# Performance work log

Hardware: AMD Instinct MI355X
Metric: run time of the kernel (lower is better)

## Reference

```python
import math
import jax, jax.numpy as jnp
import numpy as np

B, N, L, E, H, T = 64, 8, 128, 768, 12, 64


def setup_inputs() -> dict:
    key = jax.random.key(0)
    ks = jax.random.split(key, 8)
    s = 0.02
    return {
        "x":  jax.random.normal(ks[0], (B, N, L, E), dtype=jnp.float32),
        # torch Linear weights are [out, in]
        "Wq": jax.random.normal(ks[1], (H, E, E), dtype=jnp.float32) * s,
        "bq": jax.random.normal(ks[2], (H, E), dtype=jnp.float32) * s,
        "Wv": jax.random.normal(ks[3], (H, T, E), dtype=jnp.float32) * s,
        "bv": jax.random.normal(ks[4], (H, T), dtype=jnp.float32) * s,
        "Wf": jax.random.normal(ks[5], (E, H * T), dtype=jnp.float32) * s,
        "bf": jax.random.normal(ks[6], (E,), dtype=jnp.float32) * s,
    }


def reference(x, Wq, bq, Wv, bv, Wf, bf):
    b, n, l, e = x.shape
    S = b * n                      # set_size after the view(-1, L, E)
    x2 = x.reshape(S, l, e)
    # per-head query projection (batched over heads)
    Q = jnp.einsum('sle,hfe->hslf', x2, Wq) + bq[:, None, None, :]      # [H,S,L,E]
    # raw (unsoftmaxed) attention: (Q K^T) V / sqrt(E)
    scores = jnp.einsum('hslf,smf->hslm', Q, x2)                        # [H,S,L,L]
    attn = jnp.einsum('hslm,sme->hsle', scores, x2) * (1.0 / math.sqrt(e))
    # per-head value projection to transformer_dim
    V = jnp.einsum('hsle,hte->hslt', attn, Wv) + bv[:, None, None, :]   # [H,S,L,T]
    # concat heads along last dim (head order preserved)
    cat = jnp.transpose(V, (1, 2, 0, 3)).reshape(S, l, -1)              # [S,L,H*T]
    out = cat @ Wf.T + bf                                               # [S,L,E]
    return out.reshape(b, n, l, e)
```

## Files before the change

kernel.cpp:

```cpp
#include <hip/hip_runtime.h>
#include <stdint.h>


#define EE 768
#define SLOT 50331648L

typedef short s16x8 __attribute__((ext_vector_type(8)));
typedef float f32x4 __attribute__((ext_vector_type(4)));

__device__ __forceinline__ short f2bf(float f){
  union { float fv; uint32_t u; } v; v.fv = f;
  uint32_t r = (v.u + 0x7fffu + ((v.u >> 16) & 1u)) >> 16;
  return (short)r;
}

__device__ __forceinline__ void gld_lds16(const short* g, short* l){
  __builtin_amdgcn_global_load_lds(
      (const __attribute__((address_space(1))) void*)(uintptr_t)g,
      (__attribute__((address_space(3))) void*)(uintptr_t)l,
      16, 0, 0);
}

__device__ __forceinline__ int xcd_swz(int bid, int nwg){
  int xcd = bid & 7, loc = bid >> 3;
  int q = nwg >> 3, r = nwg & 7;
  return (xcd < r ? xcd * (q + 1) : r * (q + 1) + (xcd - r) * q) + loc;
}

__device__ __forceinline__ int swz64(int row, int c){ return c ^ ((row & 7) << 3); }
__device__ __forceinline__ int swz32(int row, int c){ return c ^ (((row >> 1) & 3) << 3); }

__global__ __launch_bounds__(256) void cast_bf16_k(const float* __restrict__ src,
                                                   short* __restrict__ dst,
                                                   long n, float scale){
  long i = ((long)blockIdx.x * 256 + threadIdx.x) * 8;
  if(i >= n) return;
  float4 a = *(const float4*)(src + i);
  float4 b = *(const float4*)(src + i + 4);
  s16x8 o;
  o[0]=f2bf(a.x*scale); o[1]=f2bf(a.y*scale); o[2]=f2bf(a.z*scale); o[3]=f2bf(a.w*scale);
  o[4]=f2bf(b.x*scale); o[5]=f2bf(b.y*scale); o[6]=f2bf(b.z*scale); o[7]=f2bf(b.w*scale);
  *(s16x8*)(dst + i) = o;
}

__global__ __launch_bounds__(256) void cvec_k(const float* __restrict__ Wf,
                                              const float* __restrict__ bv,
                                              const float* __restrict__ bfv,
                                              float* __restrict__ c){
  int e = blockIdx.x * 256 + threadIdx.x;
  if(e >= EE) return;
  float s = bfv[e];
  for(int k = 0; k < EE; ++k) s += Wf[(long)e * EE + k] * bv[k];
  c[e] = s;
}

__global__ __launch_bounds__(256) void bias_build(const float* __restrict__ bq,
                                                  float* __restrict__ biasQP){
  int i = blockIdx.x * 256 + threadIdx.x;
  if(i < 9984) biasQP[i] = (i < 9216) ? bq[i] : 0.f;
}

__global__ __launch_bounds__(512, 1) void gemm256(const short* __restrict__ A,
                                                  const short* __restrict__ W,
                                                  const float* __restrict__ bias,
                                                  short* __restrict__ OutBase,
                                                  int hBase, int nSub, int pSub){
  __shared__ short lds[2][16384];
  const int tid = threadIdx.x, lane = tid & 63, w = tid >> 6;
  const int wr = w >> 2, wc = w & 3;
  const int bid = xcd_swz(blockIdx.x, nSub * 768);
  const int g = bid / 768, rb = bid - g * 768;
  const int rowBlk = rb / 3, colBlk = rb - rowBlk * 3;
  const long rowA0 = (long)rowBlk * 256;
  const int colB0 = colBlk * 256;
  const int wh = (g == pSub) ? 12 : hBase + g;
  const short* Bm = W + (long)wh * 589824L;
  short* Out = OutBase + (long)g * SLOT;

  const int sr0 = w * 32 + (lane >> 2);
  const int sr1 = sr0 + 16;
  const int scol = (lane & 3) * 8;
  const int sc0 = swz32(sr0, scol);
  const int sc1 = swz32(sr1, scol);
  const short* Ar0 = A + (rowA0 + sr0) * 768;
  const short* Ar1 = A + (rowA0 + sr1) * 768;
  const short* Br0 = Bm + (long)(colB0 + sr0) * 768;
  const short* Br1 = Bm + (long)(colB0 + sr1) * 768;

  f32x4 acc[8][4] = {};
  s16x8 af[4], bf0[2], bf1[2];
  const int fr = lane & 15, fc = (lane >> 4) * 8;

  auto stage = [&](int b, int kt){
    short* Al = &lds[b][0];
    short* Bl = &lds[b][8192];
    gld_lds16(Ar0 + kt + sc0, Al + (w * 2) * 512);
    gld_lds16(Ar1 + kt + sc1, Al + (w * 2 + 1) * 512);
    gld_lds16(Br0 + kt + sc0, Bl + (w * 2) * 512);
    gld_lds16(Br1 + kt + sc1, Bl + (w * 2 + 1) * 512);
  };

  stage(0, 0);
  for(int t = 0; t < 24; ++t){
    if(t < 23){
      stage((t + 1) & 1, (t + 1) * 32);
      asm volatile("s_waitcnt vmcnt(4)\n\ts_barrier" ::: "memory");
    } else {
      asm volatile("s_waitcnt vmcnt(0)\n\ts_barrier" ::: "memory");
    }
    const short* Al = &lds[t & 1][0];
    const short* Bl = &lds[t & 1][8192];

    auto loadA = [&](int mh){
      #pragma unroll
      for(int m = 0; m < 4; ++m){
        int row = wr * 128 + (mh * 4 + m) * 16 + fr;
        af[m] = *(const s16x8*)&Al[row * 32 + swz32(row, fc)];
      }
    };
    auto loadB = [&](int nh, s16x8* bf){
      #pragma unroll
      for(int n = 0; n < 2; ++n){
        int row = wc * 64 + (nh * 2 + n) * 16 + fr;
        bf[n] = *(const s16x8*)&Bl[row * 32 + swz32(row, fc)];
      }
    };
    auto mm = [&](int mh, int nh, s16x8* bf){
      __builtin_amdgcn_s_setprio(1);
      #pragma unroll
      for(int m = 0; m < 4; ++m)
        #pragma unroll
        for(int n = 0; n < 2; ++n)
          acc[mh * 4 + m][nh * 2 + n] = __builtin_amdgcn_mfma_f32_16x16x32_bf16(
              af[m], bf[n], acc[mh * 4 + m][nh * 2 + n], 0, 0, 0);
      __builtin_amdgcn_s_setprio(0);
    };

    loadA(0); loadB(0, bf0); mm(0, 0, bf0);
    loadB(1, bf1);           mm(0, 1, bf1);
    loadA(1);                mm(1, 1, bf1);
    loadB(0, bf0);           mm(1, 0, bf0);
    asm volatile("s_barrier" ::: "memory");
  }

  float bb[4];
  #pragma unroll
  for(int n = 0; n < 4; ++n)
    bb[n] = bias[wh * 768 + colB0 + wc * 64 + n * 16 + fr];

  short* Cs = &lds[0][0];
  #pragma unroll
  for(int ch = 0; ch < 2; ++ch){
    __syncthreads();
    if(wr == ch){
      #pragma unroll
      for(int m = 0; m < 8; ++m)
        #pragma unroll
        for(int n = 0; n < 4; ++n)
          #pragma unroll
          for(int r2 = 0; r2 < 4; ++r2){
            int row = m * 16 + (lane >> 4) * 4 + r2;
            int c = wc * 64 + n * 16 + fr;
            Cs[row * 256 + (c ^ (((row >> 2) & 3) << 4))] = f2bf(acc[m][n][r2] + bb[n]);
          }
    }
    __syncthreads();
    #pragma unroll
    for(int i = 0; i < 8; ++i){
      int idx = i * 512 + tid;
      int row = idx >> 5, cl = (idx & 31) * 8;
      s16x8 v = *(const s16x8*)&Cs[row * 256 + (cl ^ (((row >> 2) & 3) << 4))];
      *(s16x8*)&Out[(rowA0 + ch * 128 + row) * 768 + colB0 + cl] = v;
    }
  }
}

__global__ __launch_bounds__(256, 2) void gemm_f32(const short* __restrict__ A,
                                                   const short* __restrict__ B,
                                                   const float* __restrict__ bias,
                                                   float* __restrict__ Cout){
  __shared__ short smem[4 * 8192];
  const int tid = threadIdx.x, lane = tid & 63, w = tid >> 6;
  const int wr = w >> 1, wc = w & 1;
  const int nCol = 6;
  const int xcd = blockIdx.x & 7, loc = blockIdx.x >> 3;
  const int width = nCol << 3;
  const int gid = loc / width, rem = loc % width;
  const int rowBlk = (xcd << 6) + (gid << 3) + (rem & 7);
  const int colBlk = rem >> 3;
  const long rowA0 = (long)rowBlk << 7;
  const long colB0 = (long)colBlk << 7;
  const int lr = lane >> 3;
  const int sA = swz64(lr, (lane & 7) * 8);

  f32x4 acc[4][4] = {};
  auto stage = [&](int b, int kt){
    short* As = smem + b * 16384;
    #pragma unroll
    for(int it = 0; it < 4; ++it){
      int r = it * 32 + w * 8;
      gld_lds16(&A[(rowA0 + r + lr) * 768 + kt + sA], &As[r * 64]);
      gld_lds16(&B[(colB0 + r + lr) * 768 + kt + sA], &As[8192 + r * 64]);
    }
  };

  stage(0, 0);
  for(int t = 0; t < 12; ++t){
    const int cur = t & 1;
    if(t < 11){
      stage(cur ^ 1, (t + 1) * 64);
      asm volatile("s_waitcnt vmcnt(8)\n\ts_barrier" ::: "memory");
    } else {
      asm volatile("s_waitcnt vmcnt(0)\n\ts_barrier" ::: "memory");
    }
    const short* As = smem + cur * 16384;
    const short* Bs = As + 8192;
    #pragma unroll
    for(int kk = 0; kk < 2; ++kk){
      s16x8 af[4], bfr[4];
      #pragma unroll
      for(int m = 0; m < 4; ++m){
        int row = wr * 64 + m * 16 + (lane & 15);
        af[m] = *(const s16x8*)&As[row * 64 + swz64(row, kk * 32 + (lane >> 4) * 8)];
      }
      #pragma unroll
      for(int n = 0; n < 4; ++n){
        int row = wc * 64 + n * 16 + (lane & 15);
        bfr[n] = *(const s16x8*)&Bs[row * 64 + swz64(row, kk * 32 + (lane >> 4) * 8)];
      }
      #pragma unroll
      for(int m = 0; m < 4; ++m)
        #pragma unroll
        for(int n = 0; n < 4; ++n)
          acc[m][n] = __builtin_amdgcn_mfma_f32_16x16x32_bf16(af[m], bfr[n], acc[m][n], 0, 0, 0);
    }
    asm volatile("s_barrier" ::: "memory");
  }

  const long crow0 = rowA0 + wr * 64;
  const long ccol0 = colB0 + wc * 64;
  #pragma unroll
  for(int n = 0; n < 4; ++n){
    const long col = ccol0 + n * 16 + (lane & 15);
    const float bbv = bias[col];
    #pragma unroll
    for(int m = 0; m < 4; ++m)
      #pragma unroll
      for(int r = 0; r < 4; ++r){
        const long row = crow0 + m * 16 + (lane >> 4) * 4 + r;
        Cout[row * 768 + col] = acc[m][n][r] + bbv;
      }
  }
}

__global__ __launch_bounds__(256, 2) void attn_k(const short* __restrict__ Q,
                                                 const short* __restrict__ P,
                                                 const short* __restrict__ X,
                                                 short* __restrict__ Cat,
                                                 int h0, int nH){
  __shared__ short smem[4 * 8192];
  const int tid = threadIdx.x, lane = tid & 63, w = tid >> 6;
  const int wr = w >> 1, wc = w & 1;
  const int nwg = nH << 9;
  const int bid = xcd_swz(blockIdx.x, nwg);
  const int s = bid / nH, hi = bid - s * nH, h = h0 + hi;
  const long row0 = (long)s * 128;
  const int lr = lane >> 3;
  const int sA = swz64(lr, (lane & 7) * 8);

  const int pm = tid >> 3, pt0 = (tid & 7) * 8;
  s16x8 pv[4];
  #pragma unroll
  for(int i = 0; i < 4; ++i)
    pv[i] = *(const s16x8*)&P[(row0 + pm + i * 32) * 768L + h * 64 + pt0];

  f32x4 acc[4][4] = {};
  const short* Qh = Q + (long)hi * SLOT;
  auto stage = [&](int b, int kt){
    short* As = smem + b * 16384;
    #pragma unroll
    for(int it = 0; it < 4; ++it){
      int r = it * 32 + w * 8;
      gld_lds16(&Qh[(row0 + r + lr) * 768L + kt + sA], &As[r * 64]);
      gld_lds16(&X[(row0 + r + lr) * 768L + kt + sA], &As[8192 + r * 64]);
    }
  };

  stage(0, 0);
  for(int t = 0; t < 12; ++t){
    const int cur = t & 1;
    if(t < 11){
      stage(cur ^ 1, (t + 1) * 64);
      asm volatile("s_waitcnt vmcnt(8)\n\ts_barrier" ::: "memory");
    } else {
      asm volatile("s_waitcnt vmcnt(0)\n\ts_barrier" ::: "memory");
    }
    const short* As = smem + cur * 16384;
    const short* Bs = As + 8192;
    #pragma unroll
    for(int kk = 0; kk < 2; ++kk){
      s16x8 af[4], bfr[4];
      #pragma unroll
      for(int m = 0; m < 4; ++m){
        int row = wr * 64 + m * 16 + (lane & 15);
        af[m] = *(const s16x8*)&As[row * 64 + swz64(row, kk * 32 + (lane >> 4) * 8)];
      }
      #pragma unroll
      for(int n = 0; n < 4; ++n){
        int row = wc * 64 + n * 16 + (lane & 15);
        bfr[n] = *(const s16x8*)&Bs[row * 64 + swz64(row, kk * 32 + (lane >> 4) * 8)];
      }
      #pragma unroll
      for(int m = 0; m < 4; ++m)
        #pragma unroll
        for(int n = 0; n < 4; ++n)
          acc[m][n] = __builtin_amdgcn_mfma_f32_16x16x32_bf16(af[m], bfr[n], acc[m][n], 0, 0, 0);
    }
    asm volatile("s_barrier" ::: "memory");
  }

  short* Pt = smem;
  short* Vt = smem + 8192;
  short* Ss = smem + 16384;

  #pragma unroll
  for(int m = 0; m < 4; ++m)
    #pragma unroll
    for(int n = 0; n < 4; ++n)
      #pragma unroll
      for(int r = 0; r < 4; ++r){
        int row = wr * 64 + m * 16 + (lane >> 4) * 4 + r;
        int c = wc * 64 + n * 16 + (lane & 15);
        Ss[row * 128 + swz64(row, c)] = f2bf(acc[m][n][r]);
      }
  #pragma unroll
  for(int i = 0; i < 4; ++i)
    #pragma unroll
    for(int j = 0; j < 8; ++j){
      int trow = pt0 + j;
      int mc = pm + i * 32;
      Pt[trow * 128 + swz64(trow, mc)] = pv[i][j];
    }
  __syncthreads();

  f32x4 accv[2][4] = {};
  #pragma unroll
  for(int kk = 0; kk < 4; ++kk){
    s16x8 a2[2], b4[4];
    #pragma unroll
    for(int m = 0; m < 2; ++m){
      int row = w * 32 + m * 16 + (lane & 15);
      a2[m] = *(const s16x8*)&Ss[row * 128 + swz64(row, kk * 32 + (lane >> 4) * 8)];
    }
    #pragma unroll
    for(int n = 0; n < 4; ++n){
      int trow = n * 16 + (lane & 15);
      b4[n] = *(const s16x8*)&Pt[trow * 128 + swz64(trow, kk * 32 + (lane >> 4) * 8)];
    }
    #pragma unroll
    for(int m = 0; m < 2; ++m)
      #pragma unroll
      for(int n = 0; n < 4; ++n)
        accv[m][n] = __builtin_amdgcn_mfma_f32_16x16x32_bf16(a2[m], b4[n], accv[m][n], 0, 0, 0);
  }

  #pragma unroll
  for(int m = 0; m < 2; ++m)
    #pragma unroll
    for(int n = 0; n < 4; ++n)
      #pragma unroll
      for(int r = 0; r < 4; ++r){
        int row = w * 32 + m * 16 + (lane >> 4) * 4 + r;
        int c = n * 16 + (lane & 15);
        Vt[row * 64 + swz64(row, c)] = f2bf(accv[m][n][r]);
      }
  __syncthreads();
  #pragma unroll
  for(int k2 = 0; k2 < 4; ++k2){
    int row = k2 * 32 + (tid >> 3);
    int cl = (tid & 7) * 8;
    s16x8 v = *(const s16x8*)&Vt[row * 64 + swz64(row, cl)];
    *(s16x8*)&Cat[(row0 + row) * 768L + h * 64 + cl] = v;
  }
}

extern "C" void kernel_launch(void* const* d_in, const int* in_sizes, int n_in,
                              void* d_out, int out_size, void* d_ws, size_t ws_size,
                              hipStream_t stream){
  const float* x  = (const float*)d_in[0];
  const float* Wq = (const float*)d_in[1];
  const float* bq = (const float*)d_in[2];
  const float* Wv = (const float*)d_in[3];
  const float* bv = (const float*)d_in[4];
  const float* Wf = (const float*)d_in[5];
  const float* bfv= (const float*)d_in[6];

  const float rsqE = 0.03608439182435161f;
  char* ws = (char*)d_ws;

  short* Xb  = (short*)(ws);
  short* Cat = (short*)(ws + 100663296L);
  short* Wb  = (short*)(ws + 201326592L);
  short* Wfb = (short*)(ws + 216662016L);
  float* bQP = (float*)(ws + 217841664L);
  float* cv  = (float*)(ws + 217881600L);
  short* QS  = (short*)(ws + 217884672L);

  const size_t QOFF = 217884672ULL;
  int G = 1;
  const int cands[5] = {12, 6, 4, 3, 2};
  for(int i = 0; i < 5; ++i)
    if(ws_size >= QOFF + (size_t)(cands[i] + 1) * 100663296ULL){ G = cands[i]; break; }
  short* Pall = QS + (long)G * SLOT;

  dim3 b256(256), b512(512);
  cast_bf16_k<<<24576, b256, 0, stream>>>(x,  Xb, 50331648L, 1.f);
  cast_bf16_k<<<3456,  b256, 0, stream>>>(Wq, Wb, 7077888L, 1.f);
  cast_bf16_k<<<288,   b256, 0, stream>>>(Wv, Wb + 7077888L, 589824L, rsqE);
  cast_bf16_k<<<288,   b256, 0, stream>>>(Wf, Wfb, 589824L, 1.f);
  bias_build<<<39, b256, 0, stream>>>(bq, bQP);
  cvec_k<<<3, b256, 0, stream>>>(Wf, bv, bfv, cv);

  const int nB = 12 / G;
  for(int b = 0; b < nB; ++b){
    const int nSub = G + (b == 0 ? 1 : 0);
    const int pSub = (b == 0) ? G : -1;
    gemm256<<<dim3(nSub * 768), b512, 0, stream>>>(Xb, Wb, bQP, QS, b * G, nSub, pSub);
    attn_k<<<dim3(G * 512), b256, 0, stream>>>(QS, Pall, Xb, Cat, b * G, G);
  }
  gemm_f32<<<dim3(3072), b256, 0, stream>>>(Cat, Wfb, cv, (float*)d_out);
}
```

Baseline: 1.740 ms.

## Add 4-stage LDS-pipelined 256x256 GEMM with phased MFMA for projections

```diff
diff --git a/kernel.cpp b/kernel.cpp
--- a/kernel.cpp
+++ b/kernel.cpp
@@ -58,6 +58,142 @@
                                                   float* __restrict__ biasQP){
   int i = blockIdx.x * 256 + threadIdx.x;
   if(i < 9984) biasQP[i] = (i < 9216) ? bq[i] : 0.f;
+}
+
+template<bool OUTF32>
+__global__ __launch_bounds__(512, 1) void gemm8ph(const short* __restrict__ A,
+                                                  const short* __restrict__ W,
+                                                  const float* __restrict__ bias,
+                                                  void* __restrict__ OutBase,
+                                                  int hBase, int nSub, int pSub){
+  extern __shared__ short lds[];
+  const int tid = threadIdx.x, lane = tid & 63, w = tid >> 6;
+  const int wr = w >> 2, wc = w & 3;
+  const int bid = xcd_swz(blockIdx.x, nSub * 768);
+  const int g = bid / 768, rb = bid - g * 768;
+  const int rowBlk = rb / 3, colBlk = rb - rowBlk * 3;
+  const long rowA0 = (long)rowBlk * 256;
+  const int colB0 = colBlk * 256;
+  const int wh = (g == pSub) ? 12 : hBase + g;
+  const short* Bm = W + (long)wh * 589824L;
+
+  const int slr = w * 16 + (lane >> 2);
+  const int scol = swz32(slr, (lane & 3) * 8);
+  const short* gA0 = A + (rowA0 + slr) * 768 + scol;
+  const short* gA1 = A + (rowA0 + 128 + slr) * 768 + scol;
+  const short* gB0 = Bm + (long)(colB0 + slr) * 768 + scol;
+  const short* gB1 = Bm + (long)(colB0 + 128 + slr) * 768 + scol;
+
+  auto stageA = [&](int kt){
+    short* Al = lds + (kt & 3) * 16384;
+    gld_lds16(gA0 + kt * 32, Al + (w * 16) * 32);
+    gld_lds16(gA1 + kt * 32, Al + (128 + w * 16) * 32);
+  };
+  auto stageB = [&](int kt){
+    short* Bl = lds + (kt & 3) * 16384 + 8192;
+    gld_lds16(gB0 + kt * 32, Bl + (w * 16) * 32);
+    gld_lds16(gB1 + kt * 32, Bl + (128 + w * 16) * 32);
+  };
+
+  f32x4 acc[8][4] = {};
+  const int fr = lane & 15, fc = (lane >> 4) * 8;
+
+  stageA(0); stageB(0); stageA(1); stageB(1); stageA(2); stageB(2);
+  asm volatile("s_waitcnt vmcnt(8)\n\ts_barrier" ::: "memory");
+
+  for(int t = 0; t < 24; ++t){
+    const short* Al = lds + (t & 3) * 16384;
+    const short* Bl = Al + 8192;
+    s16x8 bfr[4], af[4];
+    #pragma unroll
+    for(int n = 0; n < 4; ++n){
+      int row = wc * 64 + n * 16 + fr;
+      bfr[n] = *(const s16x8*)&Bl[row * 32 + swz32(row, fc)];
+    }
+    #pragma unroll
+    for(int m = 0; m < 4; ++m){
+      int row = wr * 128 + m * 16 + fr;
+      af[m] = *(const s16x8*)&Al[row * 32 + swz32(row, fc)];
+    }
+    if(t < 21) stageA(t + 3);
+    asm volatile("s_barrier" ::: "memory");
+    __builtin_amdgcn_s_setprio(1);
+    #pragma unroll
+    for(int m = 0; m < 4; ++m)
+      #pragma unroll
+      for(int n = 0; n < 4; ++n)
+        acc[m][n] = __builtin_amdgcn_mfma_f32_16x16x32_bf16(af[m], bfr[n], acc[m][n], 0, 0, 0);
+    __builtin_amdgcn_s_setprio(0);
+    asm volatile("s_barrier" ::: "memory");
+    #pragma unroll
+    for(int m = 0; m < 4; ++m){
+      int row = wr * 128 + 64 + m * 16 + fr;
+      af[m] = *(const s16x8*)&Al[row * 32 + swz32(row, fc)];
+    }
+    if(t < 21) stageB(t + 3);
+    if(t < 21)       asm volatile("s_waitcnt vmcnt(8)" ::: "memory");
+    else if(t == 21) asm volatile("s_waitcnt vmcnt(4)" ::: "memory");
+    else             asm volatile("s_waitcnt vmcnt(0)" ::: "memory");
+    asm volatile("s_barrier" ::: "memory");
+    __builtin_amdgcn_s_setprio(1);
+    #pragma unroll
+    for(int m = 0; m < 4; ++m)
+      #pragma unroll
+      for(int n = 0; n < 4; ++n)
+        acc[4 + m][n] = __builtin_amdgcn_mfma_f32_16x16x32_bf16(af[m], bfr[n], acc[4 + m][n], 0, 0, 0);
+    __builtin_amdgcn_s_setprio(0);
+    asm volatile("s_barrier" ::: "memory");
+  }
+
+  asm volatile("s_waitcnt vmcnt(0) lgkmcnt(0)" ::: "memory");
+  __syncthreads();
+
+  float bb[4];
+  #pragma unroll
+  for(int n = 0; n < 4; ++n)
+    bb[n] = bias[wh * 768 + colB0 + wc * 64 + n * 16 + fr];
+
+  if constexpr(!OUTF32){
+    short* Out = (short*)OutBase + (long)g * SLOT;
+    short* Cs = lds;
+    #pragma unroll
+    for(int ch = 0; ch < 2; ++ch){
+      __syncthreads();
+      if(wr == ch){
+        #pragma unroll
+        for(int m = 0; m < 8; ++m)
+          #pragma unroll
+          for(int n = 0; n < 4; ++n)
+            #pragma unroll
+            for(int r2 = 0; r2 < 4; ++r2){
+              int row = m * 16 + (lane >> 4) * 4 + r2;
+              int c = wc * 64 + n * 16 + fr;
+              Cs[row * 256 + (c ^ (((row >> 2) & 3) << 4))] = f2bf(acc[m][n][r2] + bb[n]);
+            }
+      }
+      __syncthreads();
+      #pragma unroll
+      for(int i = 0; i < 8; ++i){
+        int idx = i * 512 + tid;
+        int row = idx >> 5, cl = (idx & 31) * 8;
+        s16x8 v = *(const s16x8*)&Cs[row * 256 + (cl ^ (((row >> 2) & 3) << 4))];
+        *(s16x8*)&Out[(rowA0 + ch * 128 + row) * 768 + colB0 + cl] = v;
+      }
+    }
+  } else {
+    float* Co = (float*)OutBase;
+    const long crow0 = rowA0 + wr * 128;
+    #pragma unroll
+    for(int mf = 0; mf < 8; ++mf)
+      #pragma unroll
+      for(int n = 0; n < 4; ++n)
+        #pragma unroll
+        for(int r2 = 0; r2 < 4; ++r2){
+          const long row = crow0 + mf * 16 + (lane >> 4) * 4 + r2;
+          const int col = colB0 + wc * 64 + n * 16 + fr;
+          Co[row * 768 + col] = acc[mf][n][r2] + bb[n];
+        }
+  }
 }
 
 __global__ __launch_bounds__(512, 1) void gemm256(const short* __restrict__ A,
@@ -413,6 +549,12 @@
     if(ws_size >= QOFF + (size_t)(cands[i] + 1) * 100663296ULL){ G = cands[i]; break; }
   short* Pall = QS + (long)G * SLOT;
 
+  bool deep =
+      hipFuncSetAttribute(reinterpret_cast<const void*>(&gemm8ph<false>),
+                          hipFuncAttributeMaxDynamicSharedMemorySize, 131072) == hipSuccess &&
+      hipFuncSetAttribute(reinterpret_cast<const void*>(&gemm8ph<true>),
+                          hipFuncAttributeMaxDynamicSharedMemorySize, 131072) == hipSuccess;
+
   dim3 b256(256), b512(512);
   cast_bf16_k<<<24576, b256, 0, stream>>>(x,  Xb, 50331648L, 1.f);
   cast_bf16_k<<<3456,  b256, 0, stream>>>(Wq, Wb, 7077888L, 1.f);
@@ -425,8 +567,14 @@
   for(int b = 0; b < nB; ++b){
     const int nSub = G + (b == 0 ? 1 : 0);
     const int pSub = (b == 0) ? G : -1;
-    gemm256<<<dim3(nSub * 768), b512, 0, stream>>>(Xb, Wb, bQP, QS, b * G, nSub, pSub);
+    if(deep)
+      gemm8ph<false><<<dim3(nSub * 768), b512, 131072, stream>>>(Xb, Wb, bQP, QS, b * G, nSub, pSub);
+    else
+      gemm256<<<dim3(nSub * 768), b512, 0, stream>>>(Xb, Wb, bQP, QS, b * G, nSub, pSub);
     attn_k<<<dim3(G * 512), b256, 0, stream>>>(QS, Pall, Xb, Cat, b * G, G);
   }
-  gemm_f32<<<dim3(3072), b256, 0, stream>>>(Cat, Wfb, cv, (float*)d_out);
-}
+  if(deep)
+    gemm8ph<true><<<dim3(768), b512, 131072, stream>>>(Cat, Wfb, cv, d_out, 0, 1, -1);
+  else
+    gemm_f32<<<dim3(3072), b256, 0, stream>>>(Cat, Wfb, cv, (float*)d_out);
+}
```

Result: no change. 1.765 ms (+1.5%).
